# Performance work log

Hardware: AMD Instinct MI355X
Metric: run time of the kernel (lower is better)

The kernel has to match this reference:

```python
import jax, jax.numpy as jnp
import numpy as np

EPS = 1e-6

def _ste(x, xq):
    return x + jax.lax.stop_gradient(xq - x)

def rmsnorm(x, w):
    return x * jax.lax.rsqrt(jnp.mean(x * x, axis=-1, keepdims=True) + EPS) * w

def act_quant(x):
    # per-token absmax int8 quantization (BitNet b1.58)
    s = 127.0 / jnp.clip(jnp.max(jnp.abs(x), axis=-1, keepdims=True), 1e-5)
    return _ste(x, jnp.clip(jnp.round(x * s), -128, 127) / s)

def w_quant(w):
    # per-tensor mean-absmax ternary quantization
    s = 1.0 / jnp.clip(jnp.mean(jnp.abs(w)), 1e-5)
    return _ste(w, jnp.clip(jnp.round(w * s), -1, 1) / s)

def bitlinear(x, w):
    return act_quant(x) @ w_quant(w).T

def snake_beta(x, log_a, log_b):
    a = jnp.exp(log_a)
    b = jnp.exp(log_b)
    s = jnp.sin(a * x)
    return x + (1.0 / (b + 1e-9)) * s * s

def ffn(x, nw, w1, la, lb, w2):
    h = bitlinear(rmsnorm(x, nw), w1)
    return bitlinear(snake_beta(h, la, lb), w2)

def mha(x, nw, ipw, ipb, opw, opb, num_heads):
    B, T, D = x.shape
    hd = D // num_heads
    xn = rmsnorm(x, nw)
    qkv = xn @ ipw.T + ipb  # [B,T,3D]
    q, k, v = jnp.split(qkv, 3, axis=-1)
    def heads(t):
        return t.reshape(B, T, num_heads, hd).transpose(0, 2, 1, 3)  # [B,H,T,hd]
    q, k, v = heads(q), heads(k), heads(v)
    scores = jnp.einsum('bhqd,bhkd->bhqk', q, k) / jnp.sqrt(jnp.asarray(hd, x.dtype))
    attn = jax.nn.softmax(scores, axis=-1)
    o = jnp.einsum('bhqk,bhkd->bhqd', attn, v)
    o = o.transpose(0, 2, 1, 3).reshape(B, T, D)
    return o @ opw.T + opb

def conv_branch(x, nw, pw1, dw, dwb, bg, bb, bm, bv, la, lb, pw2, K):
    B, T, D = x.shape
    h = rmsnorm(x, nw)
    h = bitlinear(h, pw1)  # [B,T,2D] (1x1 BitConv1d)
    a, g = jnp.split(h, 2, axis=-1)
    h = a * jax.nn.sigmoid(g)  # GLU over channels
    hc = h.transpose(0, 2, 1)  # [B,D,T]
    hc = jax.lax.conv_general_dilated(
        hc, dw, window_strides=(1,), padding=[(K // 2, K // 2)],
        feature_group_count=D, dimension_numbers=('NCH', 'OIH', 'NCH'))
    hc = hc + dwb[None, :, None]
    hc = (hc - bm[None, :, None]) * jax.lax.rsqrt(bv[None, :, None] + 1e-5) * bg[None, :, None] + bb[None, :, None]
    h = hc.transpose(0, 2, 1)  # [B,T,D]
    h = snake_beta(h, la, lb)
    return bitlinear(h, pw2)

def setup_inputs() -> dict:
    key = jax.random.key(0)
    B, T, D, H, K = 4, 2048, 512, 8, 31
    ks = jax.random.split(key, 16)
    n = lambda k, s: (jax.random.normal(k, s, jnp.float32) * 0.02)
    d = {
        'x': jax.random.normal(ks[0], (B, T, D), jnp.float32),
        'ff1_norm_w': jnp.ones((D,), jnp.float32),
        'ff1_w1': n(ks[1], (4 * D, D)), 'ff1_a': jnp.zeros((4 * D,), jnp.float32),
        'ff1_b': jnp.zeros((4 * D,), jnp.float32), 'ff1_w2': n(ks[2], (D, 4 * D)),
        'attn_norm_w': jnp.ones((D,), jnp.float32),
        'in_proj_w': n(ks[3], (3 * D, D)), 'in_proj_b': jnp.zeros((3 * D,), jnp.float32),
        'out_proj_w': n(ks[4], (D, D)), 'out_proj_b': jnp.zeros((D,), jnp.float32),
        'conv_norm_w': jnp.ones((D,), jnp.float32),
        'pw1_w': n(ks[5], (2 * D, D)),
        'dw_w': n(ks[6], (D, 1, K)), 'dw_b': jnp.zeros((D,), jnp.float32),
        'bn_g': jnp.ones((D,), jnp.float32), 'bn_b': jnp.zeros((D,), jnp.float32),
        'bn_m': jnp.zeros((D,), jnp.float32), 'bn_v': jnp.ones((D,), jnp.float32),
        'snake_a': jnp.zeros((D,), jnp.float32), 'snake_b': jnp.zeros((D,), jnp.float32),
        'pw2_w': n(ks[7], (D, D)),
        'ff2_norm_w': jnp.ones((D,), jnp.float32),
        'ff2_w1': n(ks[8], (4 * D, D)), 'ff2_a': jnp.zeros((4 * D,), jnp.float32),
        'ff2_b': jnp.zeros((4 * D,), jnp.float32), 'ff2_w2': n(ks[9], (D, 4 * D)),
        'final_norm_w': jnp.ones((D,), jnp.float32),
    }
    return d

def reference(x, ff1_norm_w, ff1_w1, ff1_a, ff1_b, ff1_w2, attn_norm_w, in_proj_w, in_proj_b, out_proj_w, out_proj_b, conv_norm_w, pw1_w, dw_w, dw_b, bn_g, bn_b, bn_m, bn_v, snake_a, snake_b, pw2_w, ff2_norm_w, ff2_w1, ff2_a, ff2_b, ff2_w2, final_norm_w):
    H, K = 8, 31
    x = x + 0.5 * ffn(x, ff1_norm_w, ff1_w1, ff1_a, ff1_b, ff1_w2)
    x = x + mha(x, attn_norm_w, in_proj_w, in_proj_b, out_proj_w, out_proj_b, H)
    x = x + conv_branch(x, conv_norm_w, pw1_w, dw_w, dw_b, bn_g, bn_b, bn_m, bn_v, snake_a, snake_b, pw2_w, K)
    x = x + 0.5 * ffn(x, ff2_norm_w, ff2_w1, ff2_a, ff2_b, ff2_w2)
    return rmsnorm(x, final_norm_w)
```

## Files before the change

kernel.cpp:

```cpp
#include <hip/hip_runtime.h>
#include <math.h>


typedef int   v4i __attribute__((ext_vector_type(4)));
typedef float v4f __attribute__((ext_vector_type(4)));
typedef float v16f __attribute__((ext_vector_type(16)));
typedef short v8s __attribute__((ext_vector_type(8)));
typedef unsigned short u16;

#define GLOAD_LDS(g, l) __builtin_amdgcn_global_load_lds( \
    (const __attribute__((address_space(1))) void*)(g),   \
    (__attribute__((address_space(3))) void*)(l), 16, 0, 0)

__device__ __forceinline__ float blk_sum256(float v, float* sm) {
#pragma unroll
  for (int m = 32; m; m >>= 1) v += __shfl_xor(v, m);
  int w = threadIdx.x >> 6;
  __syncthreads();
  if ((threadIdx.x & 63) == 0) sm[w] = v;
  __syncthreads();
  return sm[0] + sm[1] + sm[2] + sm[3];
}

__device__ __forceinline__ u16 f2bf(float f) {
  union { float f; unsigned u; } x;
  x.f = f;
  unsigned r = x.u + 0x7fffu + ((x.u >> 16) & 1u);
  return (u16)(r >> 16);
}

__device__ __forceinline__ float bf2f(u16 u) {
  union { unsigned u; float f; } x;
  x.u = ((unsigned)u) << 16;
  return x.f;
}

__device__ __forceinline__ void xcd_tiles(int& tx, int& ty) {
  int nx = gridDim.x;
  int flat = blockIdx.y * nx + blockIdx.x;
  int nwg = nx * gridDim.y;
  int cpx = nwg >> 3;
  int swz = (flat & 7) * cpx + (flat >> 3);
  ty = swz / nx;
  tx = swz - ty * nx;
}

__global__ __launch_bounds__(256) void wabs_stage1(
    const float* __restrict__ w0, const float* __restrict__ w1,
    const float* __restrict__ w2, const float* __restrict__ w3,
    const float* __restrict__ w4, const float* __restrict__ w5,
    float* __restrict__ part) {
  __shared__ float sm[4];
  const float* ws[6] = {w0, w1, w2, w3, w4, w5};
  const int ns[6] = {1048576, 1048576, 524288, 262144, 1048576, 1048576};
  int widx = blockIdx.x >> 6;
  int chunk = blockIdx.x & 63;
  const float* w = ws[widx];
  int n = ns[widx];
  float s = 0.f;
  for (int i = chunk * 256 + threadIdx.x; i < n; i += 64 * 256) s += fabsf(w[i]);
  s = blk_sum256(s, sm);
  if (threadIdx.x == 0) part[widx * 64 + chunk] = s;
}

__global__ __launch_bounds__(256) void wquant_all(
    const float* __restrict__ w0, const float* __restrict__ w1,
    const float* __restrict__ w2, const float* __restrict__ w3,
    const float* __restrict__ w4, const float* __restrict__ w5,
    const float* __restrict__ part, float* __restrict__ scales,
    signed char* __restrict__ out) {
  const float* ws[6] = {w0, w1, w2, w3, w4, w5};
  const int ns[6] = {1048576, 1048576, 524288, 262144, 1048576, 1048576};
  const int offs[6] = {0, 1048576, 2097152, 2621440, 2883584, 3932160};
  int widx = blockIdx.y;
  const float* w = ws[widx];
  int n = ns[widx];
  signed char* o = out + offs[widx];
  float ssum = 0.f;
#pragma unroll 8
  for (int i = 0; i < 64; ++i) ssum += part[widx * 64 + i];
  float wsc = fmaxf(ssum / (float)n, 1e-5f);
  if (blockIdx.x == 0 && threadIdx.x == 0) scales[widx] = wsc;
  float s = 1.0f / wsc;
  for (int i = blockIdx.x * 256 + threadIdx.x; i < n; i += 128 * 256)
    o[i] = (signed char)(int)fminf(fmaxf(rintf(w[i] * s), -1.f), 1.f);
}

__global__ __launch_bounds__(256) void wcvt_tabs(
    const float* __restrict__ ip, const float* __restrict__ op, u16* __restrict__ wb,
    const float* __restrict__ a1, const float* __restrict__ b1,
    const float* __restrict__ a2, const float* __restrict__ b2,
    float* __restrict__ tabs) {
  int bid = blockIdx.x;
  if (bid < 1024) {
    int i = bid * 256 + threadIdx.x;
    float4 f;
    if (i < 196608) f = *(const float4*)(ip + (size_t)i * 4);
    else f = *(const float4*)(op + (size_t)(i - 196608) * 4);
    u16* dst = wb + (size_t)i * 4;
    dst[0] = f2bf(f.x); dst[1] = f2bf(f.y); dst[2] = f2bf(f.z); dst[3] = f2bf(f.w);
  } else {
    int i = (bid - 1024) * 256 + threadIdx.x;
    if (i < 2048) {
      tabs[i] = __expf(a1[i]);
      tabs[2048 + i] = 1.0f / (__expf(b1[i]) + 1e-9f);
      tabs[4096 + i] = __expf(a2[i]);
      tabs[6144 + i] = 1.0f / (__expf(b2[i]) + 1e-9f);
    }
  }
}

__global__ __launch_bounds__(256) void rmsnorm_f32x(
    const float* __restrict__ x, const float* __restrict__ w,
    signed char* __restrict__ out8, u16* __restrict__ xbf,
    float* __restrict__ dq) {
  const int tid = threadIdx.x;
  const int lane = tid & 63, wv = tid >> 6;
  const int row = blockIdx.x * 4 + wv;
  const int c0 = lane * 8;
  const float* xr = x + (size_t)row * 512 + c0;
  float4 f0 = *(const float4*)xr;
  float4 f1 = *(const float4*)(xr + 4);
  float fin[8] = {f0.x, f0.y, f0.z, f0.w, f1.x, f1.y, f1.z, f1.w};
  v8s xb;
  float v[8];
  float ss = 0.f;
#pragma unroll
  for (int j = 0; j < 8; ++j) {
    u16 b = f2bf(fin[j]);
    xb[j] = (short)b;
    v[j] = bf2f(b);
    ss = fmaf(v[j], v[j], ss);
  }
  *(v8s*)(xbf + (size_t)row * 512 + c0) = xb;
#pragma unroll
  for (int m = 1; m < 64; m <<= 1) ss += __shfl_xor(ss, m);
  float sc = 1.0f / sqrtf(ss * (1.0f / 512.0f) + 1e-6f);
  float4 w0 = *(const float4*)(w + c0);
  float4 w1 = *(const float4*)(w + c0 + 4);
  float wv8[8] = {w0.x, w0.y, w0.z, w0.w, w1.x, w1.y, w1.z, w1.w};
  float y[8];
  float am = 0.f;
#pragma unroll
  for (int j = 0; j < 8; ++j) {
    y[j] = v[j] * sc * wv8[j];
    am = fmaxf(am, fabsf(y[j]));
  }
#pragma unroll
  for (int m = 1; m < 64; m <<= 1) am = fmaxf(am, __shfl_xor(am, m));
  float amc = fmaxf(am, 1e-5f);
  float s = 127.0f / amc;
  unsigned long long pkt = 0;
#pragma unroll
  for (int j = 0; j < 8; ++j) {
    int q = (int)rintf(y[j] * s);
    pkt |= ((unsigned long long)(unsigned char)(signed char)q) << (8 * j);
  }
  *(unsigned long long*)(out8 + (size_t)row * 512 + c0) = pkt;
  if (lane == 0) dq[row] = amc * (1.0f / 127.0f);
}

__global__ __launch_bounds__(256) void rmsnorm_wave(
    const u16* __restrict__ x, const float* __restrict__ w, int mode,
    float* __restrict__ outf, signed char* __restrict__ out8,
    u16* __restrict__ outb, float* __restrict__ dq) {
  const int tid = threadIdx.x;
  const int lane = tid & 63, wv = tid >> 6;
  const int row = blockIdx.x * 4 + wv;
  const int c0 = lane * 8;
  v8s xv = *(const v8s*)(x + (size_t)row * 512 + c0);
  float v[8];
  float ss = 0.f;
#pragma unroll
  for (int j = 0; j < 8; ++j) {
    v[j] = bf2f((u16)xv[j]);
    ss = fmaf(v[j], v[j], ss);
  }
#pragma unroll
  for (int m = 1; m < 64; m <<= 1) ss += __shfl_xor(ss, m);
  float sc = 1.0f / sqrtf(ss * (1.0f / 512.0f) + 1e-6f);
  float4 w0 = *(const float4*)(w + c0);
  float4 w1 = *(const float4*)(w + c0 + 4);
  float wv8[8] = {w0.x, w0.y, w0.z, w0.w, w1.x, w1.y, w1.z, w1.w};
  float y[8];
#pragma unroll
  for (int j = 0; j < 8; ++j) y[j] = v[j] * sc * wv8[j];
  if (mode == 0) {
    float* o = outf + (size_t)row * 512 + c0;
    *(float4*)o = make_float4(y[0], y[1], y[2], y[3]);
    *(float4*)(o + 4) = make_float4(y[4], y[5], y[6], y[7]);
  } else if (mode == 1) {
    float am = 0.f;
#pragma unroll
    for (int j = 0; j < 8; ++j) am = fmaxf(am, fabsf(y[j]));
#pragma unroll
    for (int m = 1; m < 64; m <<= 1) am = fmaxf(am, __shfl_xor(am, m));
    float amc = fmaxf(am, 1e-5f);
    float s = 127.0f / amc;
    unsigned long long pkt = 0;
#pragma unroll
    for (int j = 0; j < 8; ++j) {
      int q = (int)rintf(y[j] * s);
      pkt |= ((unsigned long long)(unsigned char)(signed char)q) << (8 * j);
    }
    *(unsigned long long*)(out8 + (size_t)row * 512 + c0) = pkt;
    if (lane == 0) dq[row] = amc * (1.0f / 127.0f);
  } else {
    v8s o;
#pragma unroll
    for (int j = 0; j < 8; ++j) o[j] = (short)f2bf(y[j]);
    *(v8s*)(outb + (size_t)row * 512 + c0) = o;
  }
}

__global__ __launch_bounds__(256) void rq2048_wave(
    const u16* __restrict__ h, signed char* __restrict__ out, float* __restrict__ dq) {
  const int tid = threadIdx.x;
  const int lane = tid & 63, wv = tid >> 6;
  const int row = blockIdx.x * 4 + wv;
  const u16* hr = h + (size_t)row * 2048;
  float vals[32];
  float am = 0.f;
#pragma unroll
  for (int g = 0; g < 4; ++g) {
    int c0 = g * 512 + lane * 8;
    v8s hv = *(const v8s*)(hr + c0);
#pragma unroll
    for (int j = 0; j < 8; ++j) {
      float v = bf2f((u16)hv[j]);
      vals[g * 8 + j] = v;
      am = fmaxf(am, fabsf(v));
    }
  }
#pragma unroll
  for (int m = 1; m < 64; m <<= 1) am = fmaxf(am, __shfl_xor(am, m));
  float amc = fmaxf(am, 1e-5f);
  float s = 127.0f / amc;
#pragma unroll
  for (int g = 0; g < 4; ++g) {
    unsigned long long pkt = 0;
#pragma unroll
    for (int j = 0; j < 8; ++j) {
      int q = (int)rintf(vals[g * 8 + j] * s);
      pkt |= ((unsigned long long)(unsigned char)(signed char)q) << (8 * j);
    }
    *(unsigned long long*)(out + (size_t)row * 2048 + g * 512 + lane * 8) = pkt;
  }
  if (lane == 0) dq[row] = amc * (1.0f / 127.0f);
}

__global__ __launch_bounds__(256) void rowquant_wave(
    const u16* __restrict__ in, signed char* __restrict__ out, float* __restrict__ dq) {
  const int tid = threadIdx.x;
  const int lane = tid & 63, wv = tid >> 6;
  const int row = blockIdx.x * 4 + wv;
  const int c0 = lane * 8;
  v8s xv = *(const v8s*)(in + (size_t)row * 512 + c0);
  float v[8];
  float am = 0.f;
#pragma unroll
  for (int j = 0; j < 8; ++j) {
    v[j] = bf2f((u16)xv[j]);
    am = fmaxf(am, fabsf(v[j]));
  }
#pragma unroll
  for (int m = 1; m < 64; m <<= 1) am = fmaxf(am, __shfl_xor(am, m));
  float amc = fmaxf(am, 1e-5f);
  float s = 127.0f / amc;
  unsigned long long pkt = 0;
#pragma unroll
  for (int j = 0; j < 8; ++j) {
    int q = (int)rintf(v[j] * s);
    pkt |= ((unsigned long long)(unsigned char)(signed char)q) << (8 * j);
  }
  *(unsigned long long*)(out + (size_t)row * 512 + c0) = pkt;
  if (lane == 0) dq[row] = amc * (1.0f / 127.0f);
}

template <int BN, int OM>
__global__ __launch_bounds__(256) void gemm_i8_t(
    const signed char* __restrict__ A, const signed char* __restrict__ B,
    const float* __restrict__ wsp, const float* __restrict__ adq,
    const u16* __restrict__ resid, float rscale,
    u16* __restrict__ outb, int N, int K,
    const float* __restrict__ ta, const float* __restrict__ tb) {
  constexpr int JF = BN / 32;
  __shared__ signed char As[16384];
  __shared__ signed char Bs[BN * 128];
  const int tid = threadIdx.x;
  int txc, tyc;
  xcd_tiles(txc, tyc);
  const int m0 = tyc << 7;
  const int n0 = txc * BN;
  const int lane = tid & 63;
  const int wv = tid >> 6;
  const int wr = (wv >> 1) << 6, wc = (wv & 1) * (16 * JF);
  const int r15 = lane & 15, khi = lane >> 4;
  const int srow = tid >> 3;
  const int sslot = (tid & 7) ^ (srow & 7);
  const signed char* Ag = A + (size_t)(m0 + srow) * K + sslot * 16;
  const signed char* Bg = B + (size_t)(n0 + srow) * K + sslot * 16;
  const size_t row32 = (size_t)32 * K;

  int aoff[4][2], boff[JF][2];
#pragma unroll
  for (int i = 0; i < 4; ++i) {
    int r = wr + i * 16 + r15;
#pragma unroll
    for (int s = 0; s < 2; ++s)
      aoff[i][s] = r * 128 + (((s << 2) + khi) ^ (r & 7)) * 16;
  }
#pragma unroll
  for (int j = 0; j < JF; ++j) {
    int c = wc + j * 16 + r15;
#pragma unroll
    for (int s = 0; s < 2; ++s)
      boff[j][s] = c * 128 + (((s << 2) + khi) ^ (c & 7)) * 16;
  }
  v4i acc[4][JF] = {};
  for (int k0 = 0; k0 < K; k0 += 128) {
    __syncthreads();
#pragma unroll
    for (int c = 0; c < 4; ++c)
      GLOAD_LDS(Ag + c * row32 + k0, As + c * 4096 + tid * 16);
#pragma unroll
    for (int c = 0; c < BN / 32; ++c)
      GLOAD_LDS(Bg + c * row32 + k0, Bs + c * 4096 + tid * 16);
    __syncthreads();
    v4i a[4][2], b[JF][2];
#pragma unroll
    for (int i = 0; i < 4; ++i) {
      a[i][0] = *(const v4i*)(As + aoff[i][0]);
      a[i][1] = *(const v4i*)(As + aoff[i][1]);
    }
#pragma unroll
    for (int j = 0; j < JF; ++j) {
      b[j][0] = *(const v4i*)(Bs + boff[j][0]);
      b[j][1] = *(const v4i*)(Bs + boff[j][1]);
    }
#pragma unroll
    for (int i = 0; i < 4; ++i)
#pragma unroll
      for (int j = 0; j < JF; ++j) {
        acc[i][j] = __builtin_amdgcn_mfma_i32_16x16x64_i8(a[i][0], b[j][0], acc[i][j], 0, 0, 0);
        acc[i][j] = __builtin_amdgcn_mfma_i32_16x16x64_i8(a[i][1], b[j][1], acc[i][j], 0, 0, 0);
      }
  }
  const float wsc = *wsp;
#pragma unroll
  for (int i = 0; i < 4; ++i) {
    int rb = m0 + wr + i * 16 + (khi << 2);
    float dqv[4];
#pragma unroll
    for (int rr = 0; rr < 4; ++rr) dqv[rr] = adq[rb + rr] * wsc;
#pragma unroll
    for (int j = 0; j < JF; ++j) {
      int col = n0 + wc + j * 16 + r15;
      float sa, sib;
      if constexpr (OM == 2) { sa = ta[col]; sib = tb[col]; }
#pragma unroll
      for (int rr = 0; rr < 4; ++rr) {
        size_t idx = (size_t)(rb + rr) * N + col;
        float v = (float)acc[i][j][rr] * dqv[rr];
        if constexpr (OM == 0) {
          outb[idx] = f2bf(v);
        } else if constexpr (OM == 1) {
          outb[idx] = f2bf(fmaf(rscale, v, bf2f(resid[idx])));
        } else {
          float sn = __sinf(sa * v);
          outb[idx] = f2bf(v + sn * sn * sib);
        }
      }
    }
  }
}

template <int BN, int OM>
__global__ __launch_bounds__(256) void gemm_bf16_t(
    const u16* __restrict__ A, const u16* __restrict__ B,
    const float* __restrict__ bias, const u16* __restrict__ resid,
    u16* __restrict__ outb, int N, int K) {
  constexpr int JF = BN / 32;
  __shared__ signed char As[8192];
  __shared__ signed char Bs[BN * 64];
  const int tid = threadIdx.x;
  int txc, tyc;
  xcd_tiles(txc, tyc);
  const int m0 = tyc << 7;
  const int n0 = txc * BN;
  const int lane = tid & 63;
  const int wv = tid >> 6;
  const int wr = (wv >> 1) << 6, wc = (wv & 1) * (16 * JF);
  const int r15 = lane & 15, khi = lane >> 4;
  const int srow = tid >> 2;
  const int sslot = (tid & 3) ^ ((srow >> 1) & 3);
  const int K2 = K * 2;
  const signed char* Ag = (const signed char*)A + (size_t)(m0 + srow) * K2 + sslot * 16;
  const signed char* Bg = (const signed char*)B + (size_t)(n0 + srow) * K2 + sslot * 16;
  const size_t half = (size_t)64 * K2;

  int aoff[4], boff[JF];
#pragma unroll
  for (int i = 0; i < 4; ++i) {
    int r = wr + i * 16 + r15;
    aoff[i] = r * 64 + ((khi ^ ((r >> 1) & 3)) << 4);
  }
#pragma unroll
  for (int j = 0; j < JF; ++j) {
    int c = wc + j * 16 + r15;
    boff[j] = c * 64 + ((khi ^ ((c >> 1) & 3)) << 4);
  }
  v4f acc[4][JF] = {};
  for (int kb = 0; kb < K2; kb += 64) {
    __syncthreads();
    GLOAD_LDS(Ag + kb, As + tid * 16);
    GLOAD_LDS(Ag + half + kb, As + 4096 + tid * 16);
    GLOAD_LDS(Bg + kb, Bs + tid * 16);
    if constexpr (BN == 128) GLOAD_LDS(Bg + half + kb, Bs + 4096 + tid * 16);
    __syncthreads();
    v8s a[4], b[JF];
#pragma unroll
    for (int i = 0; i < 4; ++i) a[i] = *(const v8s*)(As + aoff[i]);
#pragma unroll
    for (int j = 0; j < JF; ++j) b[j] = *(const v8s*)(Bs + boff[j]);
#pragma unroll
    for (int i = 0; i < 4; ++i)
#pragma unroll
      for (int j = 0; j < JF; ++j)
        acc[i][j] = __builtin_amdgcn_mfma_f32_16x16x32_bf16(a[i], b[j], acc[i][j], 0, 0, 0);
  }
#pragma unroll
  for (int i = 0; i < 4; ++i) {
    int rb = m0 + wr + i * 16 + (khi << 2);
#pragma unroll
    for (int j = 0; j < JF; ++j) {
      int col = n0 + wc + j * 16 + r15;
      float bv = bias[col];
#pragma unroll
      for (int rr = 0; rr < 4; ++rr) {
        float v = acc[i][j][rr] + bv;
        if constexpr (OM == 2) {
          int rowb = rb + rr;
          int tin = rowb & 31;
          int seg = col >> 9;
          int cc = col & 511;
          int h2 = cc >> 6, d = cc & 63;
          size_t base = ((size_t)(((rowb >> 11) * 8 + h2) * 64 + ((rowb & 2047) >> 5))) * 6144;
          size_t off;
          if (seg == 0)
            off = (size_t)(8 + (d >> 4)) * 512 + ((((d >> 3) & 1) << 5) + tin) * 8 + (d & 7);
          else if (seg == 1)
            off = (size_t)(d >> 4) * 512 + ((((d >> 3) & 1) << 5) + tin) * 8 + (d & 7);
          else
            off = (size_t)(4 + ((d >> 5) << 1) + (tin >> 4)) * 512 +
                  ((((tin >> 3) & 1) << 5) + (d & 31)) * 8 + (tin & 7);
          outb[base + off] = f2bf(v);
        } else {
          size_t idx = (size_t)(rb + rr) * N + col;
          if constexpr (OM == 0) outb[idx] = f2bf(v);
          else outb[idx] = f2bf(bf2f(resid[idx]) + v);
        }
      }
    }
  }
}

__global__ __launch_bounds__(256) void attn32(
    const u16* __restrict__ kvqp, u16* __restrict__ attno) {
  __shared__ u16 KV[2][4096];
  const int tid = threadIdx.x;
  const int lane = tid & 63;
  const int wv = tid >> 6;
  const int l31 = lane & 31;
  const int hi = lane >> 5;
  const int bh = blockIdx.y;
  const int b = bh >> 3, h = bh & 7;
  const int qt = blockIdx.x * 4 + wv;
  const int q0 = qt << 5;
  const float C = 0.18033688011112042f;

  v8s qf[4];
  {
    const u16* qb = kvqp + ((size_t)(bh * 64 + qt)) * 6144 + lane * 8;
#pragma unroll
    for (int ks = 0; ks < 4; ++ks) qf[ks] = *(const v8s*)(qb + (8 + ks) * 512);
  }
  v16f o0 = {}, o1 = {};
  float l_run = 0.f;

  const u16* tb = kvqp + ((size_t)(bh * 64)) * 6144;

  GLOAD_LDS(tb + tid * 8, &KV[0][tid * 8]);
  GLOAD_LDS(tb + 2048 + tid * 8, &KV[0][2048 + tid * 8]);
  __syncthreads();

  int cur = 0;
  for (int t = 0; t < 64; ++t) {
    if (t < 63) {
      const u16* nb = tb + (size_t)(t + 1) * 6144;
      GLOAD_LDS(nb + tid * 8, &KV[cur ^ 1][tid * 8]);
      GLOAD_LDS(nb + 2048 + tid * 8, &KV[cur ^ 1][2048 + tid * 8]);
    }
    v8s kf[4], vf[4];
#pragma unroll
    for (int ks = 0; ks < 4; ++ks) kf[ks] = *(const v8s*)(&KV[cur][ks * 512 + lane * 8]);
#pragma unroll
    for (int j = 0; j < 4; ++j) vf[j] = *(const v8s*)(&KV[cur][2048 + j * 512 + lane * 8]);

    __builtin_amdgcn_s_setprio(1);
    v16f sacc = {};
#pragma unroll
    for (int ks = 0; ks < 4; ++ks)
      sacc = __builtin_amdgcn_mfma_f32_32x32x16_bf16(kf[ks], qf[ks], sacc, 0, 0, 0);
    __builtin_amdgcn_s_setprio(0);

    float s[16];
#pragma unroll
    for (int r = 0; r < 16; ++r) s[r] = exp2f(sacc[r] * C);

    {
      float a0 = (s[0] + s[1]) + (s[2] + s[3]);
      float a1 = (s[4] + s[5]) + (s[6] + s[7]);
      float a2 = (s[8] + s[9]) + (s[10] + s[11]);
      float a3 = (s[12] + s[13]) + (s[14] + s[15]);
      float ls = (a0 + a1) + (a2 + a3);
      float tsw = ls;
      asm("v_permlane32_swap_b32 %0, %1" : "+v"(tsw), "+v"(ls));
      l_run += ls + tsw;
    }

    unsigned pk[8];
#pragma unroll
    for (int g = 0; g < 8; ++g) {
      unsigned u;
      asm("v_cvt_pk_bf16_f32 %0, %1, %2" : "=v"(u) : "v"(s[2 * g]), "v"(s[2 * g + 1]));
      pk[g] = u;
    }
    asm("v_permlane32_swap_b32 %0, %1" : "+v"(pk[2]), "+v"(pk[0]));
    asm("v_permlane32_swap_b32 %0, %1" : "+v"(pk[3]), "+v"(pk[1]));
    asm("v_permlane32_swap_b32 %0, %1" : "+v"(pk[6]), "+v"(pk[4]));
    asm("v_permlane32_swap_b32 %0, %1" : "+v"(pk[7]), "+v"(pk[5]));
    v4i w0, w1;
    w0[0] = pk[0]; w0[1] = pk[1]; w0[2] = pk[2]; w0[3] = pk[3];
    w1[0] = pk[4]; w1[1] = pk[5]; w1[2] = pk[6]; w1[3] = pk[7];
    v8s pf0 = *(v8s*)&w0;
    v8s pf1 = *(v8s*)&w1;

    __builtin_amdgcn_s_setprio(1);
    o0 = __builtin_amdgcn_mfma_f32_32x32x16_bf16(vf[0], pf0, o0, 0, 0, 0);
    o0 = __builtin_amdgcn_mfma_f32_32x32x16_bf16(vf[1], pf1, o0, 0, 0, 0);
    o1 = __builtin_amdgcn_mfma_f32_32x32x16_bf16(vf[2], pf0, o1, 0, 0, 0);
    o1 = __builtin_amdgcn_mfma_f32_32x32x16_bf16(vf[3], pf1, o1, 0, 0, 0);
    __builtin_amdgcn_s_setprio(0);

    __syncthreads();
    cur ^= 1;
  }

  float inv = 1.0f / l_run;
  u16* orow = attno + (size_t)(b * 2048 + q0 + l31) * 512 + h * 64;
#pragma unroll
  for (int dt = 0; dt < 2; ++dt) {
#pragma unroll
    for (int g = 0; g < 8; ++g) {
      int d = dt * 32 + ((2 * g) & 3) + 8 * (g >> 1) + 4 * hi;
      float a = (dt ? o1[2 * g] : o0[2 * g]) * inv;
      float bv = (dt ? o1[2 * g + 1] : o0[2 * g + 1]) * inv;
      unsigned u;
      asm("v_cvt_pk_bf16_f32 %0, %1, %2" : "=v"(u) : "v"(a), "v"(bv));
      *(unsigned*)(orow + d) = u;
    }
  }
}

__global__ __launch_bounds__(256) void dwconv_fused(
    const u16* __restrict__ g3, const float* __restrict__ dww,
    const float* __restrict__ dwb, const float* __restrict__ bng,
    const float* __restrict__ bnb, const float* __restrict__ bnm,
    const float* __restrict__ bnv, const float* __restrict__ la,
    const float* __restrict__ lb, u16* __restrict__ outp) {
  __shared__ float IN[160 * 64];
  __shared__ float WT[1984];
  __shared__ float PRM[4][64];
  const int tid = threadIdx.x;
  const int cg = blockIdx.x << 6;
  const int t0 = blockIdx.y << 7;
  const int bb = blockIdx.z;

  if (tid < 64) {
    int c = cg + tid;
    float sc = bng[c] / sqrtf(bnv[c] + 1e-5f);
    PRM[0][tid] = sc;
    PRM[1][tid] = (dwb[c] - bnm[c]) * sc + bnb[c];
    PRM[2][tid] = __expf(la[c]);
    PRM[3][tid] = 1.0f / (__expf(lb[c]) + 1e-9f);
  }
  for (int i = tid; i < 1984; i += 256) WT[i] = dww[cg * 31 + i];

#pragma unroll
  for (int p = 0; p < 5; ++p) {
    int r = p * 32 + (tid >> 3);
    int t = t0 - 16 + r;
    int c8 = (tid & 7) << 3;
    float4 lo = make_float4(0.f, 0.f, 0.f, 0.f);
    float4 hv = make_float4(0.f, 0.f, 0.f, 0.f);
    if (t >= 0 && t < 2048) {
      const u16* rp = g3 + ((size_t)(bb * 2048 + t)) * 1024 + cg + c8;
      v8s a8 = *(const v8s*)rp;
      v8s g8 = *(const v8s*)(rp + 512);
      float va[8];
#pragma unroll
      for (int j = 0; j < 8; ++j) {
        float fa = bf2f((u16)a8[j]);
        float fg = bf2f((u16)g8[j]);
        va[j] = fa / (1.f + __expf(-fg));
      }
      lo = make_float4(va[0], va[1], va[2], va[3]);
      hv = make_float4(va[4], va[5], va[6], va[7]);
    }
    *(float4*)&IN[r * 64 + c8] = lo;
    *(float4*)&IN[r * 64 + c8 + 4] = hv;
  }
  __syncthreads();

  const int ch = tid & 63;
  const int tg = tid >> 6;
  const float sc = PRM[0][ch], sh = PRM[1][ch], sa = PRM[2][ch], sib = PRM[3][ch];
  float w[31];
#pragma unroll
  for (int k = 0; k < 31; ++k) w[k] = WT[ch * 31 + k];

  for (int pass = 0; pass < 4; ++pass) {
    int tl = pass * 32 + tg * 8;
    float x[38];
#pragma unroll
    for (int i = 0; i < 38; ++i) x[i] = IN[(tl + 1 + i) * 64 + ch];
    float acc[8] = {0.f, 0.f, 0.f, 0.f, 0.f, 0.f, 0.f, 0.f};
#pragma unroll
    for (int k = 0; k < 31; ++k)
#pragma unroll
      for (int j = 0; j < 8; ++j) acc[j] = fmaf(x[k + j], w[k], acc[j]);
#pragma unroll
    for (int j = 0; j < 8; ++j) {
      float v = acc[j] * sc + sh;
      float s = __sinf(sa * v);
      v += s * s * sib;
      outp[((size_t)(bb * 2048 + t0 + tl + j)) * 512 + cg + ch] = f2bf(v);
    }
  }
}

extern "C" void kernel_launch(void* const* d_in, const int* in_sizes, int n_in,
                              void* d_out, int out_size, void* d_ws, size_t ws_size,
                              hipStream_t stream) {
  const float* x_in = (const float*)d_in[0];
  const float* ff1_norm_w = (const float*)d_in[1];
  const float* ff1_w1 = (const float*)d_in[2];
  const float* ff1_a = (const float*)d_in[3];
  const float* ff1_b = (const float*)d_in[4];
  const float* ff1_w2 = (const float*)d_in[5];
  const float* attn_norm_w = (const float*)d_in[6];
  const float* in_proj_w = (const float*)d_in[7];
  const float* in_proj_b = (const float*)d_in[8];
  const float* out_proj_w = (const float*)d_in[9];
  const float* out_proj_b = (const float*)d_in[10];
  const float* conv_norm_w = (const float*)d_in[11];
  const float* pw1_w = (const float*)d_in[12];
  const float* dw_w = (const float*)d_in[13];
  const float* dw_b = (const float*)d_in[14];
  const float* bn_g = (const float*)d_in[15];
  const float* bn_b = (const float*)d_in[16];
  const float* bn_m = (const float*)d_in[17];
  const float* bn_v = (const float*)d_in[18];
  const float* snake_a = (const float*)d_in[19];
  const float* snake_b = (const float*)d_in[20];
  const float* pw2_w = (const float*)d_in[21];
  const float* ff2_norm_w = (const float*)d_in[22];
  const float* ff2_w1 = (const float*)d_in[23];
  const float* ff2_a = (const float*)d_in[24];
  const float* ff2_b = (const float*)d_in[25];
  const float* ff2_w2 = (const float*)d_in[26];
  const float* final_norm_w = (const float*)d_in[27];
  float* out = (float*)d_out;

  char* ws = (char*)d_ws;
  u16* x_bf = (u16*)(ws + 0);
  u16* x_cur = (u16*)(ws + 8388608);
  u16* kvqp = (u16*)(ws + 41943040);
  u16* attno = (u16*)(ws + 100663296);
  u16* h_b = (u16*)(ws + 16777216);
  u16* g3b = (u16*)(ws + 16777216);
  u16* convout = (u16*)(ws + 50331648);
  signed char* a8a = (signed char*)(ws + 83886080);
  signed char* a8b = (signed char*)(ws + 88080384);
  u16* xnb = (u16*)(ws + 104857600);
  signed char* wq = (signed char*)(ws + 113246208);
  signed char* wq_w1 = wq;
  signed char* wq_w2 = wq + 1048576;
  signed char* wq_p1 = wq + 2097152;
  signed char* wq_p2 = wq + 2621440;
  signed char* wq_f21 = wq + 2883584;
  signed char* wq_f22 = wq + 3932160;
  u16* wb = (u16*)(ws + 118226944);
  u16* wb_ip = wb;
  u16* wb_op = wb + 786432;
  float* scales = (float*)(ws + 120324096);
  float* partials = (float*)(ws + 120324352);
  float* ascale = (float*)(ws + 120325888);
  float* tabs = (float*)(ws + 120358912);

  wabs_stage1<<<384, 256, 0, stream>>>(ff1_w1, ff1_w2, pw1_w, pw2_w, ff2_w1, ff2_w2, partials);
  wquant_all<<<dim3(128, 6), 256, 0, stream>>>(ff1_w1, ff1_w2, pw1_w, pw2_w, ff2_w1, ff2_w2,
                                               partials, scales, wq);
  wcvt_tabs<<<1032, 256, 0, stream>>>(in_proj_w, out_proj_w, wb, ff1_a, ff1_b, ff2_a, ff2_b,
                                      tabs);

  rmsnorm_f32x<<<2048, 256, 0, stream>>>(x_in, ff1_norm_w, a8a, x_bf, ascale);
  gemm_i8_t<128, 2><<<dim3(16, 64), 256, 0, stream>>>(
      a8a, wq_w1, scales + 0, ascale, nullptr, 1.0f, h_b, 2048, 512, tabs, tabs + 2048);
  rq2048_wave<<<2048, 256, 0, stream>>>(h_b, a8b, ascale);
  gemm_i8_t<64, 1><<<dim3(8, 64), 256, 0, stream>>>(
      a8b, wq_w2, scales + 1, ascale, x_bf, 0.5f, x_cur, 512, 2048, nullptr, nullptr);

  rmsnorm_wave<<<2048, 256, 0, stream>>>(x_cur, attn_norm_w, 2, nullptr, nullptr, xnb, nullptr);
  gemm_bf16_t<128, 2><<<dim3(12, 64), 256, 0, stream>>>(
      xnb, wb_ip, in_proj_b, nullptr, kvqp, 1536, 512);
  attn32<<<dim3(16, 32), 256, 0, stream>>>(kvqp, attno);
  gemm_bf16_t<64, 1><<<dim3(8, 64), 256, 0, stream>>>(
      attno, wb_op, out_proj_b, x_cur, x_cur, 512, 512);

  rmsnorm_wave<<<2048, 256, 0, stream>>>(x_cur, conv_norm_w, 1, nullptr, a8a, nullptr, ascale);
  gemm_i8_t<128, 0><<<dim3(8, 64), 256, 0, stream>>>(
      a8a, wq_p1, scales + 2, ascale, nullptr, 1.0f, g3b, 1024, 512, nullptr, nullptr);
  dwconv_fused<<<dim3(8, 16, 4), 256, 0, stream>>>(g3b, dw_w, dw_b, bn_g, bn_b, bn_m, bn_v,
                                                   snake_a, snake_b, convout);
  rowquant_wave<<<2048, 256, 0, stream>>>(convout, a8a, ascale);
  gemm_i8_t<64, 1><<<dim3(8, 64), 256, 0, stream>>>(
      a8a, wq_p2, scales + 3, ascale, x_cur, 1.0f, x_cur, 512, 512, nullptr, nullptr);

  rmsnorm_wave<<<2048, 256, 0, stream>>>(x_cur, ff2_norm_w, 1, nullptr, a8a, nullptr, ascale);
  gemm_i8_t<128, 2><<<dim3(16, 64), 256, 0, stream>>>(
      a8a, wq_f21, scales + 4, ascale, nullptr, 1.0f, h_b, 2048, 512, tabs + 4096, tabs + 6144);
  rq2048_wave<<<2048, 256, 0, stream>>>(h_b, a8b, ascale);
  gemm_i8_t<64, 1><<<dim3(8, 64), 256, 0, stream>>>(
      a8b, wq_f22, scales + 5, ascale, x_cur, 0.5f, x_cur, 512, 2048, nullptr, nullptr);

  rmsnorm_wave<<<2048, 256, 0, stream>>>(x_cur, final_norm_w, 0, out, nullptr, nullptr, nullptr);
}
```

Before: 292.4 us.

## Quantize QKV in-projection to int8 and swizzle attention block mapping

The attention input projection now runs through the int8 MFMA GEMM instead of bf16. in_proj weights get a per-tensor absmax int8 quantization in the weight-prep kernels, and the normed activations are quantized per row to int8. The QKV scatter layout and bias add move into a new output mode of the int8 GEMM. Attention blocks are also remapped so neighbouring workgroups share batch-head data across XCDs. This aims to cut GEMM and weight-conversion cost, but it adds quantization error to a layer the reference computes in full precision.

```diff
diff --git a/kernel.cpp b/kernel.cpp
--- a/kernel.cpp
+++ b/kernel.cpp
@@ -20,6 +20,16 @@
   if ((threadIdx.x & 63) == 0) sm[w] = v;
   __syncthreads();
   return sm[0] + sm[1] + sm[2] + sm[3];
+}
+
+__device__ __forceinline__ float blk_max256(float v, float* sm) {
+#pragma unroll
+  for (int m = 32; m; m >>= 1) v = fmaxf(v, __shfl_xor(v, m));
+  int w = threadIdx.x >> 6;
+  __syncthreads();
+  if ((threadIdx.x & 63) == 0) sm[w] = v;
+  __syncthreads();
+  return fmaxf(fmaxf(sm[0], sm[1]), fmaxf(sm[2], sm[3]));
 }
 
 __device__ __forceinline__ u16 f2bf(float f) {
@@ -49,58 +59,76 @@
     const float* __restrict__ w0, const float* __restrict__ w1,
     const float* __restrict__ w2, const float* __restrict__ w3,
     const float* __restrict__ w4, const float* __restrict__ w5,
-    float* __restrict__ part) {
+    const float* __restrict__ w6, float* __restrict__ part) {
   __shared__ float sm[4];
-  const float* ws[6] = {w0, w1, w2, w3, w4, w5};
-  const int ns[6] = {1048576, 1048576, 524288, 262144, 1048576, 1048576};
+  const float* ws[7] = {w0, w1, w2, w3, w4, w5, w6};
+  const int ns[7] = {1048576, 1048576, 524288, 262144, 1048576, 1048576, 786432};
   int widx = blockIdx.x >> 6;
   int chunk = blockIdx.x & 63;
   const float* w = ws[widx];
   int n = ns[widx];
-  float s = 0.f;
-  for (int i = chunk * 256 + threadIdx.x; i < n; i += 64 * 256) s += fabsf(w[i]);
-  s = blk_sum256(s, sm);
-  if (threadIdx.x == 0) part[widx * 64 + chunk] = s;
+  if (widx < 6) {
+    float s = 0.f;
+    for (int i = chunk * 256 + threadIdx.x; i < n; i += 64 * 256) s += fabsf(w[i]);
+    s = blk_sum256(s, sm);
+    if (threadIdx.x == 0) part[widx * 64 + chunk] = s;
+  } else {
+    float s = 0.f;
+    for (int i = chunk * 256 + threadIdx.x; i < n; i += 64 * 256) s = fmaxf(s, fabsf(w[i]));
+    s = blk_max256(s, sm);
+    if (threadIdx.x == 0) part[widx * 64 + chunk] = s;
+  }
 }
 
 __global__ __launch_bounds__(256) void wquant_all(
     const float* __restrict__ w0, const float* __restrict__ w1,
     const float* __restrict__ w2, const float* __restrict__ w3,
     const float* __restrict__ w4, const float* __restrict__ w5,
+    const float* __restrict__ w6,
     const float* __restrict__ part, float* __restrict__ scales,
     signed char* __restrict__ out) {
-  const float* ws[6] = {w0, w1, w2, w3, w4, w5};
-  const int ns[6] = {1048576, 1048576, 524288, 262144, 1048576, 1048576};
-  const int offs[6] = {0, 1048576, 2097152, 2621440, 2883584, 3932160};
+  const float* ws[7] = {w0, w1, w2, w3, w4, w5, w6};
+  const int ns[7] = {1048576, 1048576, 524288, 262144, 1048576, 1048576, 786432};
+  const int offs[7] = {0, 1048576, 2097152, 2621440, 2883584, 3932160, 4980736};
   int widx = blockIdx.y;
   const float* w = ws[widx];
   int n = ns[widx];
   signed char* o = out + offs[widx];
-  float ssum = 0.f;
+  float s, clipv;
+  if (widx < 6) {
+    float ssum = 0.f;
 #pragma unroll 8
-  for (int i = 0; i < 64; ++i) ssum += part[widx * 64 + i];
-  float wsc = fmaxf(ssum / (float)n, 1e-5f);
-  if (blockIdx.x == 0 && threadIdx.x == 0) scales[widx] = wsc;
-  float s = 1.0f / wsc;
+    for (int i = 0; i < 64; ++i) ssum += part[widx * 64 + i];
+    float wsc = fmaxf(ssum / (float)n, 1e-5f);
+    if (blockIdx.x == 0 && threadIdx.x == 0) scales[widx] = wsc;
+    s = 1.0f / wsc;
+    clipv = 1.f;
+  } else {
+    float am = 0.f;
+#pragma unroll 8
+    for (int i = 0; i < 64; ++i) am = fmaxf(am, part[widx * 64 + i]);
+    float step = fmaxf(am, 1e-5f) * (1.0f / 127.0f);
+    if (blockIdx.x == 0 && threadIdx.x == 0) scales[widx] = step;
+    s = 1.0f / step;
+    clipv = 127.f;
+  }
   for (int i = blockIdx.x * 256 + threadIdx.x; i < n; i += 128 * 256)
-    o[i] = (signed char)(int)fminf(fmaxf(rintf(w[i] * s), -1.f), 1.f);
+    o[i] = (signed char)(int)fminf(fmaxf(rintf(w[i] * s), -clipv), clipv);
 }
 
 __global__ __launch_bounds__(256) void wcvt_tabs(
-    const float* __restrict__ ip, const float* __restrict__ op, u16* __restrict__ wb,
+    const float* __restrict__ op, u16* __restrict__ wb,
     const float* __restrict__ a1, const float* __restrict__ b1,
     const float* __restrict__ a2, const float* __restrict__ b2,
     float* __restrict__ tabs) {
   int bid = blockIdx.x;
-  if (bid < 1024) {
+  if (bid < 256) {
     int i = bid * 256 + threadIdx.x;
-    float4 f;
-    if (i < 196608) f = *(const float4*)(ip + (size_t)i * 4);
-    else f = *(const float4*)(op + (size_t)(i - 196608) * 4);
+    float4 f = *(const float4*)(op + (size_t)i * 4);
     u16* dst = wb + (size_t)i * 4;
     dst[0] = f2bf(f.x); dst[1] = f2bf(f.y); dst[2] = f2bf(f.z); dst[3] = f2bf(f.w);
   } else {
-    int i = (bid - 1024) * 256 + threadIdx.x;
+    int i = (bid - 256) * 256 + threadIdx.x;
     if (i < 2048) {
       tabs[i] = __expf(a1[i]);
       tabs[2048 + i] = 1.0f / (__expf(b1[i]) + 1e-9f);
@@ -283,7 +311,8 @@
     const float* __restrict__ wsp, const float* __restrict__ adq,
     const u16* __restrict__ resid, float rscale,
     u16* __restrict__ outb, int N, int K,
-    const float* __restrict__ ta, const float* __restrict__ tb) {
+    const float* __restrict__ ta, const float* __restrict__ tb,
+    const float* __restrict__ bias) {
   constexpr int JF = BN / 32;
   __shared__ signed char As[16384];
   __shared__ signed char Bs[BN * 128];
@@ -356,19 +385,39 @@
 #pragma unroll
     for (int j = 0; j < JF; ++j) {
       int col = n0 + wc + j * 16 + r15;
-      float sa, sib;
+      float sa, sib, bv;
       if constexpr (OM == 2) { sa = ta[col]; sib = tb[col]; }
+      if constexpr (OM == 3) { bv = bias[col]; }
 #pragma unroll
       for (int rr = 0; rr < 4; ++rr) {
-        size_t idx = (size_t)(rb + rr) * N + col;
         float v = (float)acc[i][j][rr] * dqv[rr];
-        if constexpr (OM == 0) {
-          outb[idx] = f2bf(v);
-        } else if constexpr (OM == 1) {
-          outb[idx] = f2bf(fmaf(rscale, v, bf2f(resid[idx])));
+        if constexpr (OM == 3) {
+          v += bv;
+          int rowb = rb + rr;
+          int tin = rowb & 31;
+          int seg = col >> 9;
+          int cc = col & 511;
+          int h2 = cc >> 6, d = cc & 63;
+          size_t base = ((size_t)(((rowb >> 11) * 8 + h2) * 64 + ((rowb & 2047) >> 5))) * 6144;
+          size_t off;
+          if (seg == 0)
+            off = (size_t)(8 + (d >> 4)) * 512 + ((((d >> 3) & 1) << 5) + tin) * 8 + (d & 7);
+          else if (seg == 1)
+            off = (size_t)(d >> 4) * 512 + ((((d >> 3) & 1) << 5) + tin) * 8 + (d & 7);
+          else
+            off = (size_t)(4 + ((d >> 5) << 1) + (tin >> 4)) * 512 +
+                  ((((tin >> 3) & 1) << 5) + (d & 31)) * 8 + (tin & 7);
+          outb[base + off] = f2bf(v);
         } else {
-          float sn = __sinf(sa * v);
-          outb[idx] = f2bf(v + sn * sn * sib);
+          size_t idx = (size_t)(rb + rr) * N + col;
+          if constexpr (OM == 0) {
+            outb[idx] = f2bf(v);
+          } else if constexpr (OM == 1) {
+            outb[idx] = f2bf(fmaf(rscale, v, bf2f(resid[idx])));
+          } else {
+            float sn = __sinf(sa * v);
+            outb[idx] = f2bf(v + sn * sn * sib);
+          }
         }
       }
     }
@@ -438,28 +487,10 @@
       float bv = bias[col];
 #pragma unroll
       for (int rr = 0; rr < 4; ++rr) {
+        size_t idx = (size_t)(rb + rr) * N + col;
         float v = acc[i][j][rr] + bv;
-        if constexpr (OM == 2) {
-          int rowb = rb + rr;
-          int tin = rowb & 31;
-          int seg = col >> 9;
-          int cc = col & 511;
-          int h2 = cc >> 6, d = cc & 63;
-          size_t base = ((size_t)(((rowb >> 11) * 8 + h2) * 64 + ((rowb & 2047) >> 5))) * 6144;
-          size_t off;
-          if (seg == 0)
-            off = (size_t)(8 + (d >> 4)) * 512 + ((((d >> 3) & 1) << 5) + tin) * 8 + (d & 7);
-          else if (seg == 1)
-            off = (size_t)(d >> 4) * 512 + ((((d >> 3) & 1) << 5) + tin) * 8 + (d & 7);
-          else
-            off = (size_t)(4 + ((d >> 5) << 1) + (tin >> 4)) * 512 +
-                  ((((tin >> 3) & 1) << 5) + (d & 31)) * 8 + (tin & 7);
-          outb[base + off] = f2bf(v);
-        } else {
-          size_t idx = (size_t)(rb + rr) * N + col;
-          if constexpr (OM == 0) outb[idx] = f2bf(v);
-          else outb[idx] = f2bf(bf2f(resid[idx]) + v);
-        }
+        if constexpr (OM == 0) outb[idx] = f2bf(v);
+        else outb[idx] = f2bf(bf2f(resid[idx]) + v);
       }
     }
   }
@@ -473,9 +504,11 @@
   const int wv = tid >> 6;
   const int l31 = lane & 31;
   const int hi = lane >> 5;
-  const int bh = blockIdx.y;
+  const int flat = blockIdx.y * 16 + blockIdx.x;
+  const int qg = flat >> 5;
+  const int bh = (flat & 7) | (((flat >> 3) & 3) << 3);
   const int b = bh >> 3, h = bh & 7;
-  const int qt = blockIdx.x * 4 + wv;
+  const int qt = qg * 4 + wv;
   const int q0 = qt << 5;
   const float C = 0.18033688011112042f;
 
@@ -701,49 +734,51 @@
   signed char* wq_p2 = wq + 2621440;
   signed char* wq_f21 = wq + 2883584;
   signed char* wq_f22 = wq + 3932160;
-  u16* wb = (u16*)(ws + 118226944);
-  u16* wb_ip = wb;
-  u16* wb_op = wb + 786432;
+  signed char* wq_ip = wq + 4980736;
+  u16* wb = (u16*)(ws + 119013376);
+  u16* wb_op = wb;
   float* scales = (float*)(ws + 120324096);
   float* partials = (float*)(ws + 120324352);
   float* ascale = (float*)(ws + 120325888);
   float* tabs = (float*)(ws + 120358912);
 
-  wabs_stage1<<<384, 256, 0, stream>>>(ff1_w1, ff1_w2, pw1_w, pw2_w, ff2_w1, ff2_w2, partials);
-  wquant_all<<<dim3(128, 6), 256, 0, stream>>>(ff1_w1, ff1_w2, pw1_w, pw2_w, ff2_w1, ff2_w2,
-                                               partials, scales, wq);
-  wcvt_tabs<<<1032, 256, 0, stream>>>(in_proj_w, out_proj_w, wb, ff1_a, ff1_b, ff2_a, ff2_b,
-                                      tabs);
+  wabs_stage1<<<448, 256, 0, stream>>>(ff1_w1, ff1_w2, pw1_w, pw2_w, ff2_w1, ff2_w2,
+                                       in_proj_w, partials);
+  wquant_all<<<dim3(128, 7), 256, 0, stream>>>(ff1_w1, ff1_w2, pw1_w, pw2_w, ff2_w1, ff2_w2,
+                                               in_proj_w, partials, scales, wq);
+  wcvt_tabs<<<264, 256, 0, stream>>>(out_proj_w, wb, ff1_a, ff1_b, ff2_a, ff2_b, tabs);
 
   rmsnorm_f32x<<<2048, 256, 0, stream>>>(x_in, ff1_norm_w, a8a, x_bf, ascale);
   gemm_i8_t<128, 2><<<dim3(16, 64), 256, 0, stream>>>(
-      a8a, wq_w1, scales + 0, ascale, nullptr, 1.0f, h_b, 2048, 512, tabs, tabs + 2048);
+      a8a, wq_w1, scales + 0, ascale, nullptr, 1.0f, h_b, 2048, 512, tabs, tabs + 2048, nullptr);
   rq2048_wave<<<2048, 256, 0, stream>>>(h_b, a8b, ascale);
   gemm_i8_t<64, 1><<<dim3(8, 64), 256, 0, stream>>>(
-      a8b, wq_w2, scales + 1, ascale, x_bf, 0.5f, x_cur, 512, 2048, nullptr, nullptr);
-
-  rmsnorm_wave<<<2048, 256, 0, stream>>>(x_cur, attn_norm_w, 2, nullptr, nullptr, xnb, nullptr);
-  gemm_bf16_t<128, 2><<<dim3(12, 64), 256, 0, stream>>>(
-      xnb, wb_ip, in_proj_b, nullptr, kvqp, 1536, 512);
+      a8b, wq_w2, scales + 1, ascale, x_bf, 0.5f, x_cur, 512, 2048, nullptr, nullptr, nullptr);
+
+  rmsnorm_wave<<<2048, 256, 0, stream>>>(x_cur, attn_norm_w, 1, nullptr, a8a, nullptr, ascale);
+  gemm_i8_t<128, 3><<<dim3(12, 64), 256, 0, stream>>>(
+      a8a, wq_ip, scales + 6, ascale, nullptr, 1.0f, kvqp, 1536, 512, nullptr, nullptr,
+      in_proj_b);
   attn32<<<dim3(16, 32), 256, 0, stream>>>(kvqp, attno);
   gemm_bf16_t<64, 1><<<dim3(8, 64), 256, 0, stream>>>(
       attno, wb_op, out_proj_b, x_cur, x_cur, 512, 512);
 
   rmsnorm_wave<<<2048, 256, 0, stream>>>(x_cur, conv_norm_w, 1, nullptr, a8a, nullptr, ascale);
   gemm_i8_t<128, 0><<<dim3(8, 64), 256, 0, stream>>>(
-      a8a, wq_p1, scales + 2, ascale, nullptr, 1.0f, g3b, 1024, 512, nullptr, nullptr);
+      a8a, wq_p1, scales + 2, ascale, nullptr, 1.0f, g3b, 1024, 512, nullptr, nullptr, nullptr);
   dwconv_fused<<<dim3(8, 16, 4), 256, 0, stream>>>(g3b, dw_w, dw_b, bn_g, bn_b, bn_m, bn_v,
                                                    snake_a, snake_b, convout);
   rowquant_wave<<<2048, 256, 0, stream>>>(convout, a8a, ascale);
   gemm_i8_t<64, 1><<<dim3(8, 64), 256, 0, stream>>>(
-      a8a, wq_p2, scales + 3, ascale, x_cur, 1.0f, x_cur, 512, 512, nullptr, nullptr);
+      a8a, wq_p2, scales + 3, ascale, x_cur, 1.0f, x_cur, 512, 512, nullptr, nullptr, nullptr);
 
   rmsnorm_wave<<<2048, 256, 0, stream>>>(x_cur, ff2_norm_w, 1, nullptr, a8a, nullptr, ascale);
   gemm_i8_t<128, 2><<<dim3(16, 64), 256, 0, stream>>>(
-      a8a, wq_f21, scales + 4, ascale, nullptr, 1.0f, h_b, 2048, 512, tabs + 4096, tabs + 6144);
+      a8a, wq_f21, scales + 4, ascale, nullptr, 1.0f, h_b, 2048, 512, tabs + 4096, tabs + 6144,
+      nullptr);
   rq2048_wave<<<2048, 256, 0, stream>>>(h_b, a8b, ascale);
   gemm_i8_t<64, 1><<<dim3(8, 64), 256, 0, stream>>>(
-      a8b, wq_f22, scales + 5, ascale, x_cur, 0.5f, x_cur, 512, 2048, nullptr, nullptr);
+      a8b, wq_f22, scales + 5, ascale, x_cur, 0.5f, x_cur, 512, 2048, nullptr, nullptr, nullptr);
 
   rmsnorm_wave<<<2048, 256, 0, stream>>>(x_cur, final_norm_w, 0, out, nullptr, nullptr, nullptr);
 }
```

Measured after the change: 292.7 us. Within noise of the previous version (+0.1%).
